# Optimization experiments

Hardware: AMD Instinct MI355X
Metric: run time of the kernel (lower is better)

The kernel has to match this reference:

```python
import jax, jax.numpy as jnp
import numpy as np

HEADS = 6
EPS = 1e-5


def _na_idx(L, k, d):
    # NATTEN-style dilated neighborhood: work within dilation cosets,
    # clamp window to stay inside the image (window shifts at borders).
    i = np.arange(L)
    g = i % d
    p = i // d
    Lg = (L - g + d - 1) // d  # coset length per position
    start = np.clip(p - k // 2, 0, Lg - k)
    j = np.arange(k)
    nbr = g[:, None] + d * (start[:, None] + j[None, :])          # [L,k] neighbor coords
    rel = (start[:, None] + j[None, :]) - p[:, None] + (k - 1)    # [L,k] rpb index in [0,2k-2]
    return jnp.asarray(nbr, jnp.int32), jnp.asarray(rel, jnp.int32)


def _na2d(x, qkv_w, qkv_b, proj_w, proj_b, rpb, heads, k, d):
    # x: [B,H,W,C] NHWC neighborhood attention with relative positional bias
    B, H, W, C = x.shape
    dh = C // heads
    scale = dh ** -0.5
    qkv = (x @ qkv_w + qkv_b).reshape(B, H, W, 3, heads, dh)
    qkv = jnp.transpose(qkv, (3, 0, 4, 1, 2, 5))  # [3,B,h,H,W,dh]
    q, kk, v = qkv[0] * scale, qkv[1], qkv[2]
    nh, rh = _na_idx(H, k, d)
    nw, rw = _na_idx(W, k, d)

    def gather(t):  # [B,h,H,W,dh] -> [B,h,H,W,k,k,dh]
        t = t[:, :, nh]              # [B,h,H,k,W,dh]
        t = t[:, :, :, :, nw]        # [B,h,H,k,W,k,dh]
        return jnp.transpose(t, (0, 1, 2, 4, 3, 5, 6))

    kn, vn = gather(kk), gather(v)
    attn = jnp.einsum('bhxyd,bhxyijd->bhxyij', q, kn)  # [B,h,H,W,k,k]
    bias = rpb[:, rh]                  # [h,H,k,2k-1]
    bias = bias[:, :, :, rw]           # [h,H,k,W,k]
    bias = jnp.transpose(bias, (0, 1, 3, 2, 4))  # [h,H,W,k,k]
    attn = attn + bias[None]
    attn = jax.nn.softmax(attn.reshape(B, heads, H, W, k * k), axis=-1)
    attn = attn.reshape(B, heads, H, W, k, k)
    out = jnp.einsum('bhxyij,bhxyijd->bhxyd', attn, vn)
    out = jnp.transpose(out, (0, 2, 3, 1, 4)).reshape(B, H, W, C)
    return out @ proj_w + proj_b


def _rln(x, w, b, m1_w, m1_b, m2_w, m2_b):
    # Revised LayerNorm: normalize over (C,H,W) per sample; meta1/meta2 are 1x1 convs on std/mean
    mean = jnp.mean(x, axis=(1, 2, 3), keepdims=True)
    std = jnp.sqrt(jnp.mean((x - mean) ** 2, axis=(1, 2, 3), keepdims=True) + EPS)
    out = (x - mean) / std * w + b
    rescale = m1_w[None, :, None, None] * std + m1_b[None, :, None, None]
    rebias = m2_w[None, :, None, None] * mean + m2_b[None, :, None, None]
    return out, rescale, rebias


def _c11(x, w, b):  # 1x1 conv on NCHW == per-pixel linear
    return jnp.einsum('bchw,oc->bohw', x, w) + b[None, :, None, None]


def _gelu(x):
    return jax.nn.gelu(x, approximate=False)


def reference(x, ln_w, ln_b, m1_w, m1_b, m2_w, m2_b, qkv1_w, qkv1_b, proj1_w, proj1_b, rpb1, qkv2_w, qkv2_b, proj2_w, proj2_b, rpb2, mlp_w1, mlp_b1, mlp_w2, mlp_b2, bn_g, bn_b, bn_m, bn_v, pa_w1, pa_b1, pa_w2, pa_b2, ca_w1, ca_b1, ca_w2, ca_b2, m2a_w1, m2a_b1, m2a_w2, m2a_b2):
    # ---- NA block 1 (kernel 7, dilation 1) ----
    sc = x
    y, rs, rb = _rln(x, ln_w, ln_b, m1_w, m1_b, m2_w, m2_b)
    a = _na2d(jnp.transpose(y, (0, 2, 3, 1)), qkv1_w, qkv1_b, proj1_w, proj1_b, rpb1, HEADS, 7, 1)
    x = sc + jnp.transpose(a, (0, 3, 1, 2)) * rs + rb
    # ---- NA block 2 (kernel 5, dilation 8) ----
    sc = x
    y, rs, rb = _rln(x, ln_w, ln_b, m1_w, m1_b, m2_w, m2_b)
    a = _na2d(jnp.transpose(y, (0, 2, 3, 1)), qkv2_w, qkv2_b, proj2_w, proj2_b, rpb2, HEADS, 5, 8)
    x = sc + jnp.transpose(a, (0, 3, 1, 2)) * rs + rb
    # ---- MLP (source reuses the pre-attn2 shortcut `sc`) ----
    y, rs, rb = _rln(x, ln_w, ln_b, m1_w, m1_b, m2_w, m2_b)
    m = _c11(jax.nn.relu(_c11(y, mlp_w1, mlp_b1)), mlp_w2, mlp_b2)
    x = sc + m * rs + rb
    # ---- BN + pixel attention + channel attention + mlp2 ----
    sc = x
    inv = jax.lax.rsqrt(bn_v + EPS)
    y = (x - bn_m[None, :, None, None]) * (inv * bn_g)[None, :, None, None] + bn_b[None, :, None, None]
    pa = jax.nn.sigmoid(_c11(_gelu(_c11(y, pa_w1, pa_b1)), pa_w2, pa_b2))  # [B,1,H,W]
    y = pa * y
    gap = jnp.mean(y, axis=(2, 3), keepdims=True)
    ca = jax.nn.sigmoid(_c11(_gelu(_c11(gap, ca_w1, ca_b1)), ca_w2, ca_b2))  # [B,C,1,1]
    y = ca * y
    y = _c11(_gelu(_c11(y, m2a_w1, m2a_b1)), m2a_w2, m2a_b2)
    return sc + y


def setup_inputs() -> dict:
    key = jax.random.key(0)
    B, C, H, W, HID = 4, 96, 64, 64, 384
    ks = iter(jax.random.split(key, 48))

    def rn(shape, s=0.02):
        return jax.random.normal(next(ks), shape, jnp.float32) * s

    d = {}
    d['x'] = jax.random.normal(next(ks), (B, C, H, W), jnp.float32)
    d['ln_w'] = jnp.ones((1, C, 1, 1), jnp.float32)
    d['ln_b'] = jnp.zeros((1, C, 1, 1), jnp.float32)
    d['m1_w'] = rn((C,)); d['m1_b'] = jnp.ones((C,), jnp.float32)
    d['m2_w'] = rn((C,)); d['m2_b'] = jnp.zeros((C,), jnp.float32)
    d['qkv1_w'] = rn((C, 3 * C)); d['qkv1_b'] = jnp.zeros((3 * C,), jnp.float32)
    d['proj1_w'] = rn((C, C)); d['proj1_b'] = jnp.zeros((C,), jnp.float32)
    d['rpb1'] = rn((HEADS, 13, 13))
    d['qkv2_w'] = rn((C, 3 * C)); d['qkv2_b'] = jnp.zeros((3 * C,), jnp.float32)
    d['proj2_w'] = rn((C, C)); d['proj2_b'] = jnp.zeros((C,), jnp.float32)
    d['rpb2'] = rn((HEADS, 9, 9))
    d['mlp_w1'] = rn((HID, C)); d['mlp_b1'] = jnp.zeros((HID,), jnp.float32)
    d['mlp_w2'] = rn((C, HID)); d['mlp_b2'] = jnp.zeros((C,), jnp.float32)
    d['bn_g'] = jnp.ones((C,), jnp.float32); d['bn_b'] = jnp.zeros((C,), jnp.float32)
    d['bn_m'] = jnp.zeros((C,), jnp.float32); d['bn_v'] = jnp.ones((C,), jnp.float32)
    d['pa_w1'] = rn((C // 8, C)); d['pa_b1'] = jnp.zeros((C // 8,), jnp.float32)
    d['pa_w2'] = rn((1, C // 8)); d['pa_b2'] = jnp.zeros((1,), jnp.float32)
    d['ca_w1'] = rn((C, C)); d['ca_b1'] = jnp.zeros((C,), jnp.float32)
    d['ca_w2'] = rn((C, C)); d['ca_b2'] = jnp.zeros((C,), jnp.float32)
    d['m2a_w1'] = rn((C, C)); d['m2a_b1'] = jnp.zeros((C,), jnp.float32)
    d['m2a_w2'] = rn((C, C)); d['m2a_b2'] = jnp.zeros((C,), jnp.float32)
    return d
```

## Files before the change

kernel.cpp:

```cpp
#include <hip/hip_runtime.h>
#include <math.h>

#define CC 96
#define NP 4096
#define NHEADS 6
#define NELEMF 393216.0f
#define EPSF 1e-5f

typedef __attribute__((ext_vector_type(8))) short bf16x8;
typedef __attribute__((ext_vector_type(4))) float f32x4;
#define MFMA16(a,b,c) __builtin_amdgcn_mfma_f32_16x16x32_bf16(a,b,c,0,0,0)

#define WQKV1  64
#define WQKV2  (WQKV1+13824)
#define WPROJ1 (WQKV2+13824)
#define WPROJ2 (WPROJ1+4608)
#define WMLP1  (WPROJ2+4608)
#define WMLP2  (WMLP1+18432)
#define WM2A1  (WMLP2+18432)
#define WM2A2  (WM2A1+4608)
#define WPA1T  (WM2A2+4608)
#define WBNS   (WPA1T+1152)
#define WS_Q   870784
#define WS_K   (WS_Q+786432)
#define WS_V   (WS_K+786432)
#define WS_ATTPM (WS_V+786432)
#define WS_X1  (WS_ATTPM+786432)
#define WS_X2  (WS_X1+1572864)
#define WS_X3  (WS_X2+1572864)
#define WS_PA  (WS_X3+1572864)
#define WS_GAP (WS_PA+16384)
#define WS_CA  (WS_GAP+384)

__device__ __forceinline__ float gelu_f(float x){
  return 0.5f * x * (1.0f + erff(x * 0.7071067811865476f));
}
__device__ __forceinline__ float sigmoid_f(float x){
  return 1.0f / (1.0f + __expf(-x));
}
__device__ __forceinline__ unsigned short bfr(float f){
  unsigned int u = __float_as_uint(f);
  u += 0x7fffu + ((u >> 16) & 1u);
  return (unsigned short)(u >> 16);
}
__device__ __forceinline__ float bflo16(unsigned short u){ return __uint_as_float(((unsigned int)u) << 16); }
__device__ __forceinline__ float bflo(unsigned int u){ return __uint_as_float(u << 16); }
__device__ __forceinline__ float bfhi(unsigned int u){ return __uint_as_float(u & 0xffff0000u); }
__device__ __forceinline__ void get_ms(const float* st, int b, float& mean, float& inv, float& stdv){
  float s = st[b], s2 = st[4+b];
  mean = s * (1.0f/NELEMF);
  float var = fmaxf(s2 * (1.0f/NELEMF) - mean*mean, 0.0f);
  stdv = sqrtf(var + EPSF);
  inv = 1.0f / stdv;
}
__device__ __forceinline__ float ldf(const float* p, int i){ return p[i]; }
__device__ __forceinline__ float ldf(const unsigned short* p, int i){ return bflo16(p[i]); }
__device__ __forceinline__ void load4(const float* p, float4& v){ v = *(const float4*)p; }
__device__ __forceinline__ void load4(const unsigned short* p, float4& v){
  ushort4 u = *(const ushort4*)p;
  v.x = bflo16(u.x); v.y = bflo16(u.y); v.z = bflo16(u.z); v.w = bflo16(u.w);
}

__global__ void prep_stats_kernel(const float* __restrict__ x, float* __restrict__ st,
                             const float* __restrict__ q1, const float* __restrict__ q2,
                             const float* __restrict__ p1, const float* __restrict__ p2,
                             const float* __restrict__ w1, const float* __restrict__ w2,
                             const float* __restrict__ a1, const float* __restrict__ a2,
                             const float* __restrict__ pw1,
                             const float* __restrict__ bg, const float* __restrict__ bb,
                             const float* __restrict__ bm, const float* __restrict__ bv,
                             float* __restrict__ ws){
  if(blockIdx.x < 384){
    int b = blockIdx.x / CC, c = blockIdx.x % CC;
    const float* p = x + (b*CC + c)*NP;
    float s = 0.f, s2 = 0.f;
    for(int i = threadIdx.x; i < NP; i += 256){ float v = p[i]; s += v; s2 = fmaf(v, v, s2); }
    for(int off = 32; off > 0; off >>= 1){ s += __shfl_down(s, off); s2 += __shfl_down(s2, off); }
    __shared__ float ls[8];
    int wid = threadIdx.x >> 6;
    if((threadIdx.x & 63) == 0){ ls[wid] = s; ls[4+wid] = s2; }
    __syncthreads();
    if(threadIdx.x == 0){
      atomicAdd(&st[b],   ls[0]+ls[1]+ls[2]+ls[3]);
      atomicAdd(&st[4+b], ls[4]+ls[5]+ls[6]+ls[7]);
    }
    return;
  }
  int gid = (blockIdx.x - 384)*256 + threadIdx.x;
  if(gid < 27648){ int n = gid/96, c = gid%96; ((unsigned short*)(ws+WQKV1))[gid] = bfr(q1[c*288+n]); }
  else if(gid < 55296){ int g = gid-27648; int n = g/96, c = g%96; ((unsigned short*)(ws+WQKV2))[g] = bfr(q2[c*288+n]); }
  else if(gid < 64512){ int g = gid-55296; int n = g/96, c = g%96; ((unsigned short*)(ws+WPROJ1))[g] = bfr(p1[c*96+n]); }
  else if(gid < 73728){ int g = gid-64512; int n = g/96, c = g%96; ((unsigned short*)(ws+WPROJ2))[g] = bfr(p2[c*96+n]); }
  else if(gid < 110592){ int g = gid-73728; ((unsigned short*)(ws+WMLP1))[g] = bfr(w1[g]); }
  else if(gid < 147456){ int g = gid-110592; ((unsigned short*)(ws+WMLP2))[g] = bfr(w2[g]); }
  else if(gid < 156672){ int g = gid-147456; ((unsigned short*)(ws+WM2A1))[g] = bfr(a1[g]); }
  else if(gid < 165888){ int g = gid-156672; ((unsigned short*)(ws+WM2A2))[g] = bfr(a2[g]); }
  else if(gid < 167040){ int g = gid-165888; int c = g/12, h = g%12; ws[WPA1T + g] = pw1[h*96+c]; }
  else if(gid < 167136){ int c = gid-167040;
    float sc = rsqrtf(bv[c] + EPSF) * bg[c];
    ws[WBNS + c] = sc;
    ws[WBNS + 96 + c] = bb[c] - bm[c]*sc;
  }
}

template<typename AT>
__global__ void __launch_bounds__(256) gemm_qkv_kernel(
    const AT* __restrict__ xin, const float* __restrict__ st,
    const float* __restrict__ lnw, const float* __restrict__ lnb,
    const unsigned short* __restrict__ wT, const float* __restrict__ qb,
    unsigned short* __restrict__ qo, unsigned short* __restrict__ ko, unsigned short* __restrict__ vo){
  __shared__ unsigned short Atl[64*104];
  __shared__ float scl[96], ofs[96];
  int m_base = blockIdx.x*64;
  int b = m_base >> 12, pxl0 = m_base & 4095;
  float mean, inv, stdv; get_ms(st, b, mean, inv, stdv);
  int tid = threadIdx.x;
  if(tid < 96){ float s = inv*lnw[tid]; scl[tid] = s; ofs[tid] = lnb[tid] - mean*s; }
  __syncthreads();
  const AT* src = xin + (size_t)b*CC*NP + pxl0;
  for(int idx = tid; idx < 96*16; idx += 256){
    int c = idx >> 4, p4 = (idx & 15) << 2;
    float4 v; load4(src + (size_t)c*NP + p4, v);
    float s = scl[c], o = ofs[c];
    Atl[(p4+0)*104 + c] = bfr(fmaf(v.x, s, o));
    Atl[(p4+1)*104 + c] = bfr(fmaf(v.y, s, o));
    Atl[(p4+2)*104 + c] = bfr(fmaf(v.z, s, o));
    Atl[(p4+3)*104 + c] = bfr(fmaf(v.w, s, o));
  }
  __syncthreads();
  int w = tid >> 6, lane = tid & 63, ml = lane & 15, q = lane >> 4;
  const unsigned short* arow = Atl + (w*16 + ml)*104;
  bf16x8 av[3];
  #pragma unroll
  for(int ks = 0; ks < 3; ++ks) av[ks] = *(const bf16x8*)(arow + ks*32 + q*8);
  f32x4 z = {0.f,0.f,0.f,0.f};
  #pragma unroll
  for(int g = 0; g < 6; ++g){
    f32x4 acc[3] = {z, z, z};
    #pragma unroll
    for(int ks = 0; ks < 3; ++ks){
      #pragma unroll
      for(int gg = 0; gg < 3; ++gg){
        bf16x8 bv = *(const bf16x8*)(wT + (g*48 + gg*16 + ml)*96 + ks*32 + q*8);
        acc[gg] = MFMA16(av[ks], bv, acc[gg]);
      }
    }
    #pragma unroll
    for(int gg = 0; gg < 3; ++gg){
      int nfb = g*48 + gg*16;
      int t = nfb/96, head = (nfb%96) >> 4;
      float scale = (t == 0) ? 0.25f : 1.0f;
      unsigned short* dst = (t == 0) ? qo : (t == 1) ? ko : vo;
      float bias = qb[nfb + ml];
      #pragma unroll
      for(int r = 0; r < 4; ++r){
        int pxl = pxl0 + w*16 + q*4 + r;
        dst[(((size_t)(b*NHEADS + head))*NP + pxl)*16 + ml] = bfr((acc[gg][r] + bias)*scale);
      }
    }
  }
}

template<typename SCT>
__global__ void __launch_bounds__(256) gemm_proj_kernel(
    const unsigned short* __restrict__ attpm, const unsigned short* __restrict__ wT,
    const float* __restrict__ pb, const SCT* __restrict__ scx, const float* __restrict__ st,
    const float* __restrict__ m1w, const float* __restrict__ m1b,
    const float* __restrict__ m2w, const float* __restrict__ m2b,
    unsigned short* __restrict__ dst, float* __restrict__ st_out){
  int w = threadIdx.x >> 6, lane = threadIdx.x & 63;
  int ml = lane & 15, q = lane >> 4;
  int m_base = blockIdx.x*128 + w*32;
  int n0 = blockIdx.y*48;
  f32x4 acc[2][3];
  f32x4 z = {0.f,0.f,0.f,0.f};
  #pragma unroll
  for(int f=0; f<2; ++f) for(int g=0; g<3; ++g) acc[f][g] = z;
  {
    const bf16x8* a0 = (const bf16x8*)(attpm + (size_t)(m_base + ml)*96 + q*8);
    const bf16x8* a1 = (const bf16x8*)(attpm + (size_t)(m_base + 16 + ml)*96 + q*8);
    #pragma unroll
    for(int ks = 0; ks < 3; ++ks){
      bf16x8 av0 = a0[ks*4], av1 = a1[ks*4];
      #pragma unroll
      for(int g = 0; g < 3; ++g){
        bf16x8 bv = *(const bf16x8*)(wT + (n0 + g*16 + ml)*96 + ks*32 + q*8);
        acc[0][g] = MFMA16(av0, bv, acc[0][g]);
        acc[1][g] = MFMA16(av1, bv, acc[1][g]);
      }
    }
  }
  __shared__ float T[48*133];
  #pragma unroll
  for(int f = 0; f < 2; ++f)
    #pragma unroll
    for(int g = 0; g < 3; ++g)
      #pragma unroll
      for(int r = 0; r < 4; ++r)
        T[(g*16 + ml)*133 + w*32 + f*16 + q*4 + r] = acc[f][g][r];
  __syncthreads();
  int b = (blockIdx.x*128) >> 12, pxl0 = (blockIdx.x*128) & 4095;
  float mean, inv, stdv; get_ms(st, b, mean, inv, stdv);
  float s = 0.f, s2 = 0.f;
  for(int idx = threadIdx.x; idx < 48*128; idx += 256){
    int row = idx >> 7, px = idx & 127;
    int n = n0 + row;
    float rsf = fmaf(m1w[n], stdv, m1b[n]);
    float rbf = fmaf(m2w[n], mean, m2b[n]);
    int ad = (b*CC + n)*NP + pxl0 + px;
    float val = ldf(scx, ad) + (T[row*133 + px] + pb[n])*rsf + rbf;
    dst[ad] = bfr(val);
    s += val; s2 = fmaf(val, val, s2);
  }
  for(int off = 32; off > 0; off >>= 1){ s += __shfl_down(s, off); s2 += __shfl_down(s2, off); }
  __shared__ float ls[8];
  int wid = threadIdx.x >> 6;
  if((threadIdx.x & 63) == 0){ ls[wid] = s; ls[4+wid] = s2; }
  __syncthreads();
  if(threadIdx.x == 0){
    atomicAdd(&st_out[b],   ls[0]+ls[1]+ls[2]+ls[3]);
    atomicAdd(&st_out[4+b], ls[4]+ls[5]+ls[6]+ls[7]);
  }
}

__global__ void __launch_bounds__(256) gemm_mlp1_kernel(
    const unsigned short* __restrict__ xin, const float* __restrict__ st,
    const float* __restrict__ lnw, const float* __restrict__ lnb,
    const unsigned short* __restrict__ wT, const float* __restrict__ b1,
    unsigned short* __restrict__ hid){
  __shared__ unsigned short Atl[64*104];
  __shared__ float scl[96], ofs[96];
  int m_base = blockIdx.x*64;
  int b = m_base >> 12, pxl0 = m_base & 4095;
  float mean, inv, stdv; get_ms(st, b, mean, inv, stdv);
  int tid = threadIdx.x;
  if(tid < 96){ float s = inv*lnw[tid]; scl[tid] = s; ofs[tid] = lnb[tid] - mean*s; }
  __syncthreads();
  const unsigned short* src = xin + (size_t)b*CC*NP + pxl0;
  for(int idx = tid; idx < 96*16; idx += 256){
    int c = idx >> 4, p4 = (idx & 15) << 2;
    float4 v; load4(src + (size_t)c*NP + p4, v);
    float s = scl[c], o = ofs[c];
    Atl[(p4+0)*104 + c] = bfr(fmaf(v.x, s, o));
    Atl[(p4+1)*104 + c] = bfr(fmaf(v.y, s, o));
    Atl[(p4+2)*104 + c] = bfr(fmaf(v.z, s, o));
    Atl[(p4+3)*104 + c] = bfr(fmaf(v.w, s, o));
  }
  __syncthreads();
  int w = tid >> 6, lane = tid & 63, ml = lane & 15, q = lane >> 4;
  const unsigned short* arow = Atl + (w*16 + ml)*104;
  bf16x8 av[3];
  #pragma unroll
  for(int ks = 0; ks < 3; ++ks) av[ks] = *(const bf16x8*)(arow + ks*32 + q*8);
  f32x4 z = {0.f,0.f,0.f,0.f};
  #pragma unroll
  for(int g = 0; g < 8; ++g){
    f32x4 acc[3] = {z, z, z};
    #pragma unroll
    for(int ks = 0; ks < 3; ++ks){
      #pragma unroll
      for(int gg = 0; gg < 3; ++gg){
        bf16x8 bv = *(const bf16x8*)(wT + (g*48 + gg*16 + ml)*96 + ks*32 + q*8);
        acc[gg] = MFMA16(av[ks], bv, acc[gg]);
      }
    }
    #pragma unroll
    for(int gg = 0; gg < 3; ++gg){
      int n = g*48 + gg*16 + ml;
      float bias = b1[n];
      #pragma unroll
      for(int r = 0; r < 4; ++r){
        int m = m_base + w*16 + q*4 + r;
        hid[(size_t)m*384 + n] = bfr(fmaxf(acc[gg][r] + bias, 0.f));
      }
    }
  }
}

__global__ void __launch_bounds__(256) gemm_mlp2_kernel(
    const unsigned short* __restrict__ hid, const unsigned short* __restrict__ wT,
    const float* __restrict__ b2, const unsigned short* __restrict__ scx, const float* __restrict__ st,
    const float* __restrict__ m1w, const float* __restrict__ m1b,
    const float* __restrict__ m2w, const float* __restrict__ m2b,
    float* __restrict__ dst){
  int w = threadIdx.x >> 6, lane = threadIdx.x & 63;
  int ml = lane & 15, q = lane >> 4;
  int m_base = blockIdx.x*128 + w*32;
  int n0 = blockIdx.y*48;
  f32x4 acc[2][3];
  f32x4 z = {0.f,0.f,0.f,0.f};
  #pragma unroll
  for(int f=0; f<2; ++f) for(int g=0; g<3; ++g) acc[f][g] = z;
  {
    const bf16x8* a0 = (const bf16x8*)(hid + (size_t)(m_base + ml)*384 + q*8);
    const bf16x8* a1 = (const bf16x8*)(hid + (size_t)(m_base + 16 + ml)*384 + q*8);
    #pragma unroll
    for(int ks = 0; ks < 12; ++ks){
      bf16x8 av0 = a0[ks*4], av1 = a1[ks*4];
      #pragma unroll
      for(int g = 0; g < 3; ++g){
        bf16x8 bv = *(const bf16x8*)(wT + (n0 + g*16 + ml)*384 + ks*32 + q*8);
        acc[0][g] = MFMA16(av0, bv, acc[0][g]);
        acc[1][g] = MFMA16(av1, bv, acc[1][g]);
      }
    }
  }
  __shared__ float T[48*133];
  #pragma unroll
  for(int f = 0; f < 2; ++f)
    #pragma unroll
    for(int g = 0; g < 3; ++g)
      #pragma unroll
      for(int r = 0; r < 4; ++r)
        T[(g*16 + ml)*133 + w*32 + f*16 + q*4 + r] = acc[f][g][r];
  __syncthreads();
  int b = (blockIdx.x*128) >> 12, pxl0 = (blockIdx.x*128) & 4095;
  float mean, inv, stdv; get_ms(st, b, mean, inv, stdv);
  for(int idx = threadIdx.x; idx < 48*128; idx += 256){
    int row = idx >> 7, px = idx & 127;
    int n = n0 + row;
    float rsf = fmaf(m1w[n], stdv, m1b[n]);
    float rbf = fmaf(m2w[n], mean, m2b[n]);
    int ad = (b*CC + n)*NP + pxl0 + px;
    dst[ad] = ldf(scx, ad) + (T[row*133 + px] + b2[n])*rsf + rbf;
  }
}

__global__ void __launch_bounds__(256) gemm_m2a_kernel(
    const float* __restrict__ x3, const float* __restrict__ bns,
    const float* __restrict__ pa, const float* __restrict__ ca,
    const unsigned short* __restrict__ w1T, const float* __restrict__ b1,
    const unsigned short* __restrict__ w2T, const float* __restrict__ b2,
    const float* __restrict__ scx, float* __restrict__ outp){
  __shared__ __align__(16) char smbuf[26624];
  __shared__ float scl[96], ofs[96], pal[64];
  unsigned short* Atl = (unsigned short*)smbuf;
  unsigned short* tl2 = (unsigned short*)(smbuf + 13312);
  float* T = (float*)smbuf;
  int m_base = blockIdx.x*64;
  int b = m_base >> 12, pxl0 = m_base & 4095;
  int tid = threadIdx.x;
  if(tid < 96){ float cv = ca[b*96 + tid]; scl[tid] = bns[tid]*cv; ofs[tid] = bns[96+tid]*cv; }
  if(tid >= 128 && tid < 192) pal[tid-128] = pa[m_base + (tid-128)];
  __syncthreads();
  const float* src = x3 + (size_t)b*CC*NP + pxl0;
  for(int idx = tid; idx < 96*16; idx += 256){
    int c = idx >> 4, p4 = (idx & 15) << 2;
    float4 v = *(const float4*)(src + (size_t)c*NP + p4);
    float s = scl[c], o = ofs[c];
    Atl[(p4+0)*104 + c] = bfr(fmaf(v.x, s, o) * pal[p4+0]);
    Atl[(p4+1)*104 + c] = bfr(fmaf(v.y, s, o) * pal[p4+1]);
    Atl[(p4+2)*104 + c] = bfr(fmaf(v.z, s, o) * pal[p4+2]);
    Atl[(p4+3)*104 + c] = bfr(fmaf(v.w, s, o) * pal[p4+3]);
  }
  __syncthreads();
  int w = tid >> 6, lane = tid & 63, ml = lane & 15, q = lane >> 4;
  f32x4 z = {0.f,0.f,0.f,0.f};
  f32x4 acc1[6];
  #pragma unroll
  for(int g=0; g<6; ++g) acc1[g] = z;
  {
    const unsigned short* arow = Atl + (w*16 + ml)*104;
    #pragma unroll
    for(int ks = 0; ks < 3; ++ks){
      bf16x8 av = *(const bf16x8*)(arow + ks*32 + q*8);
      #pragma unroll
      for(int g = 0; g < 6; ++g){
        bf16x8 bv = *(const bf16x8*)(w1T + (g*16 + ml)*96 + ks*32 + q*8);
        acc1[g] = MFMA16(av, bv, acc1[g]);
      }
    }
  }
  #pragma unroll
  for(int g = 0; g < 6; ++g){
    float bias = b1[g*16 + ml];
    #pragma unroll
    for(int r = 0; r < 4; ++r)
      tl2[(w*16 + q*4 + r)*104 + g*16 + ml] = bfr(gelu_f(acc1[g][r] + bias));
  }
  __syncthreads();
  f32x4 acc2[6];
  #pragma unroll
  for(int g=0; g<6; ++g) acc2[g] = z;
  {
    const unsigned short* arow = tl2 + (w*16 + ml)*104;
    #pragma unroll
    for(int ks = 0; ks < 3; ++ks){
      bf16x8 av = *(const bf16x8*)(arow + ks*32 + q*8);
      #pragma unroll
      for(int g = 0; g < 6; ++g){
        bf16x8 bv = *(const bf16x8*)(w2T + (g*16 + ml)*96 + ks*32 + q*8);
        acc2[g] = MFMA16(av, bv, acc2[g]);
      }
    }
  }
  __syncthreads();
  #pragma unroll
  for(int g = 0; g < 6; ++g)
    #pragma unroll
    for(int r = 0; r < 4; ++r)
      T[(g*16 + ml)*68 + w*16 + q*4 + r] = acc2[g][r];
  __syncthreads();
  for(int idx = tid; idx < 96*64; idx += 256){
    int n = idx >> 6, p = idx & 63;
    int ad = (b*CC + n)*NP + pxl0 + p;
    outp[ad] = scx[ad] + T[n*68 + p] + b2[n];
  }
}

template<int K, int D, int RPB>
__global__ void __launch_bounds__(256) attn_kernel(
    const unsigned short* __restrict__ qb, const unsigned short* __restrict__ kb,
    const unsigned short* __restrict__ vb, const float* __restrict__ rpb,
    unsigned short* __restrict__ outp){
  int bh = blockIdx.x >> 6;
  int x = blockIdx.x & 63;
  int head = bh % NHEADS, b = bh / NHEADS;

  int gx = x % D, px = x / D;
  int Lgx = (64 - gx + D - 1) / D;
  int sx = min(max(px - K/2, 0), Lgx - K);

  __shared__ unsigned int sm[2*K*512];
  unsigned int* kl = sm;
  unsigned int* vl = sm + K*512;
  const unsigned int* kg = (const unsigned int*)(kb + (size_t)bh*NP*16);
  const unsigned int* vg = (const unsigned int*)(vb + (size_t)bh*NP*16);
  int tid = threadIdx.x;
  #pragma unroll
  for(int i = 0; i < K; ++i){
    int hh = gx + D*(sx + i);
    ((uint2*)(kl + i*512))[tid] = ((const uint2*)(kg + hh*512))[tid];
    ((uint2*)(vl + i*512))[tid] = ((const uint2*)(vg + hh*512))[tid];
  }
  __syncthreads();

  int pixoff = tid >> 2, t = tid & 3;
  int y = pixoff;
  int pix = x*64 + y;
  uint2 qd = *(const uint2*)(qb + ((size_t)bh*NP + pix)*16 + 4*t);
  float qx = bflo(qd.x), qy = bfhi(qd.x), qz = bflo(qd.y), qw = bfhi(qd.y);

  int gy = y % D, py = y / D;
  int Lgy = (64 - gy + D - 1) / D;
  int sy = min(max(py - K/2, 0), Lgy - K);

  float sc[K*K];
  #pragma unroll
  for(int i = 0; i < K; ++i){
    #pragma unroll
    for(int j = 0; j < K; ++j){
      int ww = gy + D*(sy + j);
      uint2 kv = *(const uint2*)(kl + i*512 + ww*8 + t*2);
      float s = qx*bflo(kv.x);
      s = fmaf(qy, bfhi(kv.x), s);
      s = fmaf(qz, bflo(kv.y), s);
      s = fmaf(qw, bfhi(kv.y), s);
      sc[i*K + j] = s;
    }
  }
  float mx = -1e30f;
  #pragma unroll
  for(int i = 0; i < K; ++i){
    const float* brow = rpb + (head*RPB + (sx + i - px + (K-1)))*RPB + (sy - py + (K-1));
    #pragma unroll
    for(int j = 0; j < K; ++j){
      float s = sc[i*K + j];
      s += __shfl_xor(s, 1);
      s += __shfl_xor(s, 2);
      s += brow[j];
      sc[i*K + j] = s;
      mx = fmaxf(mx, s);
    }
  }
  float sum = 0.f;
  #pragma unroll
  for(int n = 0; n < K*K; ++n){ float e = __expf(sc[n] - mx); sc[n] = e; sum += e; }
  float rs = 1.0f / sum;
  float4 acc = {0,0,0,0};
  #pragma unroll
  for(int i = 0; i < K; ++i){
    #pragma unroll
    for(int j = 0; j < K; ++j){
      int ww = gy + D*(sy + j);
      float wgt = sc[i*K + j] * rs;
      uint2 vv = *(const uint2*)(vl + i*512 + ww*8 + t*2);
      acc.x = fmaf(wgt, bflo(vv.x), acc.x);
      acc.y = fmaf(wgt, bfhi(vv.x), acc.y);
      acc.z = fmaf(wgt, bflo(vv.y), acc.z);
      acc.w = fmaf(wgt, bfhi(vv.y), acc.w);
    }
  }
  ushort4 o4;
  o4.x = bfr(acc.x); o4.y = bfr(acc.y); o4.z = bfr(acc.z); o4.w = bfr(acc.w);
  *(ushort4*)(outp + ((size_t)(b*NP + pix))*96 + head*16 + 4*t) = o4;
}

__global__ void __launch_bounds__(256) pa_kernel(
    const float* __restrict__ x3, const float* __restrict__ bns,
    const float* __restrict__ w1t, const float* __restrict__ b1,
    const float* __restrict__ w2, const float* __restrict__ b2,
    float* __restrict__ pa){
  int b = blockIdx.x >> 6;
  int px0 = (blockIdx.x & 63)*64;
  int pxq = threadIdx.x >> 2, t = threadIdx.x & 3;
  int p = px0 + pxq;
  float acc[12];
  #pragma unroll
  for(int h = 0; h < 12; ++h) acc[h] = 0.f;
  #pragma unroll 6
  for(int cc = 0; cc < 24; ++cc){
    int c = t*24 + cc;
    float yv = fmaf(x3[(b*CC + c)*NP + p], bns[c], bns[96 + c]);
    #pragma unroll
    for(int h = 0; h < 12; ++h) acc[h] = fmaf(yv, w1t[c*12 + h], acc[h]);
  }
  #pragma unroll
  for(int h = 0; h < 12; ++h){
    acc[h] += __shfl_xor(acc[h], 1);
    acc[h] += __shfl_xor(acc[h], 2);
  }
  float s = b2[0];
  #pragma unroll
  for(int h = 0; h < 12; ++h) s = fmaf(gelu_f(acc[h] + b1[h]), w2[h], s);
  if(t == 0) pa[b*NP + p] = sigmoid_f(s);
}

__global__ void gap_kernel(const float* __restrict__ x3, const float* __restrict__ bns,
                           const float* __restrict__ pa, float* __restrict__ gap){
  int b = blockIdx.x / CC, c = blockIdx.x % CC;
  float scb = bns[c], shb = bns[96 + c];
  float s = 0.f;
  for(int i = threadIdx.x; i < NP; i += 256)
    s = fmaf(fmaf(x3[(b*CC + c)*NP + i], scb, shb), pa[b*NP + i], s);
  for(int off = 32; off > 0; off >>= 1) s += __shfl_down(s, off);
  __shared__ float ls[4];
  if((threadIdx.x & 63) == 0) ls[threadIdx.x >> 6] = s;
  __syncthreads();
  if(threadIdx.x == 0) gap[blockIdx.x] = (ls[0]+ls[1]+ls[2]+ls[3]) * (1.0f/4096.0f);
}

__global__ void ca_kernel(const float* __restrict__ gap, const float* __restrict__ w1,
                          const float* __restrict__ b1, const float* __restrict__ w2,
                          const float* __restrict__ b2, float* __restrict__ ca){
  int b = blockIdx.x; int o = threadIdx.x;
  __shared__ float g[96], t[96];
  if(o < 96) g[o] = gap[b*96 + o];
  __syncthreads();
  if(o < 96){
    float a = b1[o];
    for(int c = 0; c < 96; ++c) a = fmaf(g[c], w1[o*96 + c], a);
    t[o] = gelu_f(a);
  }
  __syncthreads();
  if(o < 96){
    float a = b2[o];
    for(int c = 0; c < 96; ++c) a = fmaf(t[c], w2[o*96 + c], a);
    ca[b*96 + o] = sigmoid_f(a);
  }
}

extern "C" void kernel_launch(void* const* d_in, const int* in_sizes, int n_in,
                              void* d_out, int out_size, void* d_ws, size_t ws_size,
                              hipStream_t stream){
  (void)in_sizes; (void)n_in; (void)out_size; (void)ws_size;
  const float* x     = (const float*)d_in[0];
  const float* lnw   = (const float*)d_in[1];
  const float* lnb   = (const float*)d_in[2];
  const float* m1w   = (const float*)d_in[3];
  const float* m1b   = (const float*)d_in[4];
  const float* m2w   = (const float*)d_in[5];
  const float* m2b   = (const float*)d_in[6];
  const float* qkv1w = (const float*)d_in[7];
  const float* qkv1b = (const float*)d_in[8];
  const float* proj1w= (const float*)d_in[9];
  const float* proj1b= (const float*)d_in[10];
  const float* rpb1  = (const float*)d_in[11];
  const float* qkv2w = (const float*)d_in[12];
  const float* qkv2b = (const float*)d_in[13];
  const float* proj2w= (const float*)d_in[14];
  const float* proj2b= (const float*)d_in[15];
  const float* rpb2  = (const float*)d_in[16];
  const float* mw1   = (const float*)d_in[17];
  const float* mb1   = (const float*)d_in[18];
  const float* mw2   = (const float*)d_in[19];
  const float* mb2   = (const float*)d_in[20];
  const float* bng   = (const float*)d_in[21];
  const float* bnb   = (const float*)d_in[22];
  const float* bnm   = (const float*)d_in[23];
  const float* bnv   = (const float*)d_in[24];
  const float* paw1  = (const float*)d_in[25];
  const float* pab1  = (const float*)d_in[26];
  const float* paw2  = (const float*)d_in[27];
  const float* pab2  = (const float*)d_in[28];
  const float* caw1  = (const float*)d_in[29];
  const float* cab1  = (const float*)d_in[30];
  const float* caw2  = (const float*)d_in[31];
  const float* cab2  = (const float*)d_in[32];
  const float* aw1   = (const float*)d_in[33];
  const float* ab1   = (const float*)d_in[34];
  const float* aw2   = (const float*)d_in[35];
  const float* ab2   = (const float*)d_in[36];

  float* ws  = (float*)d_ws;
  float* out = (float*)d_out;
  float* st0 = ws;
  float* st1 = ws + 8;
  float* st2 = ws + 16;
  unsigned short* q     = (unsigned short*)(ws + WS_Q);
  unsigned short* k     = (unsigned short*)(ws + WS_K);
  unsigned short* v     = (unsigned short*)(ws + WS_V);
  unsigned short* attpm = (unsigned short*)(ws + WS_ATTPM);
  unsigned short* hid   = (unsigned short*)(ws + WS_Q);
  unsigned short* x1b   = (unsigned short*)(ws + WS_X1);
  unsigned short* x2b   = (unsigned short*)(ws + WS_X2);
  float* x3  = ws + WS_X3;
  float* pab = ws + WS_PA;
  float* gpb = ws + WS_GAP;
  float* cab = ws + WS_CA;
  float* bns = ws + WBNS;

  hipMemsetAsync(d_ws, 0, 64*sizeof(float), stream);
  prep_stats_kernel<<<1040, 256, 0, stream>>>(x, st0, qkv1w, qkv2w, proj1w, proj2w,
                                              mw1, mw2, aw1, aw2, paw1,
                                              bng, bnb, bnm, bnv, ws);

  gemm_qkv_kernel<float><<<256, 256, 0, stream>>>(x, st0, lnw, lnb,
      (unsigned short*)(ws+WQKV1), qkv1b, q, k, v);
  attn_kernel<7,1,13><<<1536, 256, 0, stream>>>(q, k, v, rpb1, attpm);
  gemm_proj_kernel<float><<<dim3(128,2), 256, 0, stream>>>(attpm, (unsigned short*)(ws+WPROJ1),
      proj1b, x, st0, m1w, m1b, m2w, m2b, x1b, st1);

  gemm_qkv_kernel<unsigned short><<<256, 256, 0, stream>>>(x1b, st1, lnw, lnb,
      (unsigned short*)(ws+WQKV2), qkv2b, q, k, v);
  attn_kernel<5,8,9><<<1536, 256, 0, stream>>>(q, k, v, rpb2, attpm);
  gemm_proj_kernel<unsigned short><<<dim3(128,2), 256, 0, stream>>>(attpm, (unsigned short*)(ws+WPROJ2),
      proj2b, x1b, st1, m1w, m1b, m2w, m2b, x2b, st2);

  gemm_mlp1_kernel<<<256, 256, 0, stream>>>(x2b, st2, lnw, lnb,
      (unsigned short*)(ws+WMLP1), mb1, hid);
  gemm_mlp2_kernel<<<dim3(128,2), 256, 0, stream>>>(hid, (unsigned short*)(ws+WMLP2), mb2,
      x1b, st2, m1w, m1b, m2w, m2b, x3);

  pa_kernel<<<256, 256, 0, stream>>>(x3, bns, ws + WPA1T, pab1, paw2, pab2, pab);
  gap_kernel<<<384, 256, 0, stream>>>(x3, bns, pab, gpb);
  ca_kernel<<<4, 128, 0, stream>>>(gpb, caw1, cab1, caw2, cab2, cab);
  gemm_m2a_kernel<<<256, 256, 0, stream>>>(x3, bns, pab, cab, (unsigned short*)(ws+WM2A1), ab1,
                                           (unsigned short*)(ws+WM2A2), ab2, x3, out);
}
```

Measured before the change: 294.0 us.

## Fuse MLP GEMMs via shared-memory hidden tile and merge PA with GAP

```diff
diff --git a/kernel.cpp b/kernel.cpp
--- a/kernel.cpp
+++ b/kernel.cpp
@@ -101,6 +101,7 @@
     ws[WBNS + c] = sc;
     ws[WBNS + 96 + c] = bb[c] - bm[c]*sc;
   }
+  else if(gid < 167520){ ws[WS_GAP + (gid-167136)] = 0.f; }
 }
 
 template<typename AT>
@@ -223,13 +224,20 @@
   }
 }
 
-__global__ void __launch_bounds__(256) gemm_mlp1_kernel(
+__global__ void __launch_bounds__(256) gemm_mlp_kernel(
     const unsigned short* __restrict__ xin, const float* __restrict__ st,
     const float* __restrict__ lnw, const float* __restrict__ lnb,
-    const unsigned short* __restrict__ wT, const float* __restrict__ b1,
-    unsigned short* __restrict__ hid){
-  __shared__ unsigned short Atl[64*104];
+    const unsigned short* __restrict__ w1T, const float* __restrict__ b1,
+    const unsigned short* __restrict__ w2T, const float* __restrict__ b2,
+    const unsigned short* __restrict__ scx,
+    const float* __restrict__ m1w, const float* __restrict__ m1b,
+    const float* __restrict__ m2w, const float* __restrict__ m2b,
+    float* __restrict__ dst){
+  __shared__ __align__(16) char smbuf[63488];
   __shared__ float scl[96], ofs[96];
+  unsigned short* Atl  = (unsigned short*)smbuf;
+  unsigned short* hidL = (unsigned short*)(smbuf + 13312);
+  float* T = (float*)(smbuf + 13312);
   int m_base = blockIdx.x*64;
   int b = m_base >> 12, pxl0 = m_base & 4095;
   float mean, inv, stdv; get_ms(st, b, mean, inv, stdv);
@@ -248,81 +256,62 @@
   }
   __syncthreads();
   int w = tid >> 6, lane = tid & 63, ml = lane & 15, q = lane >> 4;
-  const unsigned short* arow = Atl + (w*16 + ml)*104;
-  bf16x8 av[3];
-  #pragma unroll
-  for(int ks = 0; ks < 3; ++ks) av[ks] = *(const bf16x8*)(arow + ks*32 + q*8);
   f32x4 z = {0.f,0.f,0.f,0.f};
-  #pragma unroll
-  for(int g = 0; g < 8; ++g){
-    f32x4 acc[3] = {z, z, z};
-    #pragma unroll
-    for(int ks = 0; ks < 3; ++ks){
+  {
+    const unsigned short* arow = Atl + (w*16 + ml)*104;
+    bf16x8 av[3];
+    #pragma unroll
+    for(int ks = 0; ks < 3; ++ks) av[ks] = *(const bf16x8*)(arow + ks*32 + q*8);
+    #pragma unroll
+    for(int g = 0; g < 8; ++g){
+      f32x4 acc[3] = {z, z, z};
+      #pragma unroll
+      for(int ks = 0; ks < 3; ++ks){
+        #pragma unroll
+        for(int gg = 0; gg < 3; ++gg){
+          bf16x8 bv = *(const bf16x8*)(w1T + (g*48 + gg*16 + ml)*96 + ks*32 + q*8);
+          acc[gg] = MFMA16(av[ks], bv, acc[gg]);
+        }
+      }
       #pragma unroll
       for(int gg = 0; gg < 3; ++gg){
-        bf16x8 bv = *(const bf16x8*)(wT + (g*48 + gg*16 + ml)*96 + ks*32 + q*8);
-        acc[gg] = MFMA16(av[ks], bv, acc[gg]);
-      }
-    }
-    #pragma unroll
-    for(int gg = 0; gg < 3; ++gg){
-      int n = g*48 + gg*16 + ml;
-      float bias = b1[n];
-      #pragma unroll
-      for(int r = 0; r < 4; ++r){
-        int m = m_base + w*16 + q*4 + r;
-        hid[(size_t)m*384 + n] = bfr(fmaxf(acc[gg][r] + bias, 0.f));
-      }
-    }
-  }
-}
-
-__global__ void __launch_bounds__(256) gemm_mlp2_kernel(
-    const unsigned short* __restrict__ hid, const unsigned short* __restrict__ wT,
-    const float* __restrict__ b2, const unsigned short* __restrict__ scx, const float* __restrict__ st,
-    const float* __restrict__ m1w, const float* __restrict__ m1b,
-    const float* __restrict__ m2w, const float* __restrict__ m2b,
-    float* __restrict__ dst){
-  int w = threadIdx.x >> 6, lane = threadIdx.x & 63;
-  int ml = lane & 15, q = lane >> 4;
-  int m_base = blockIdx.x*128 + w*32;
-  int n0 = blockIdx.y*48;
-  f32x4 acc[2][3];
-  f32x4 z = {0.f,0.f,0.f,0.f};
-  #pragma unroll
-  for(int f=0; f<2; ++f) for(int g=0; g<3; ++g) acc[f][g] = z;
+        int n = g*48 + gg*16 + ml;
+        float bias = b1[n];
+        #pragma unroll
+        for(int r = 0; r < 4; ++r)
+          hidL[(w*16 + q*4 + r)*392 + n] = bfr(fmaxf(acc[gg][r] + bias, 0.f));
+      }
+    }
+  }
+  __syncthreads();
+  f32x4 acc2[6];
+  #pragma unroll
+  for(int g=0; g<6; ++g) acc2[g] = z;
   {
-    const bf16x8* a0 = (const bf16x8*)(hid + (size_t)(m_base + ml)*384 + q*8);
-    const bf16x8* a1 = (const bf16x8*)(hid + (size_t)(m_base + 16 + ml)*384 + q*8);
+    const unsigned short* arow = hidL + (w*16 + ml)*392;
     #pragma unroll
     for(int ks = 0; ks < 12; ++ks){
-      bf16x8 av0 = a0[ks*4], av1 = a1[ks*4];
-      #pragma unroll
-      for(int g = 0; g < 3; ++g){
-        bf16x8 bv = *(const bf16x8*)(wT + (n0 + g*16 + ml)*384 + ks*32 + q*8);
-        acc[0][g] = MFMA16(av0, bv, acc[0][g]);
-        acc[1][g] = MFMA16(av1, bv, acc[1][g]);
-      }
-    }
-  }
-  __shared__ float T[48*133];
-  #pragma unroll
-  for(int f = 0; f < 2; ++f)
-    #pragma unroll
-    for(int g = 0; g < 3; ++g)
-      #pragma unroll
-      for(int r = 0; r < 4; ++r)
-        T[(g*16 + ml)*133 + w*32 + f*16 + q*4 + r] = acc[f][g][r];
-  __syncthreads();
-  int b = (blockIdx.x*128) >> 12, pxl0 = (blockIdx.x*128) & 4095;
-  float mean, inv, stdv; get_ms(st, b, mean, inv, stdv);
-  for(int idx = threadIdx.x; idx < 48*128; idx += 256){
-    int row = idx >> 7, px = idx & 127;
-    int n = n0 + row;
+      bf16x8 av = *(const bf16x8*)(arow + ks*32 + q*8);
+      #pragma unroll
+      for(int g = 0; g < 6; ++g){
+        bf16x8 bv = *(const bf16x8*)(w2T + (g*16 + ml)*384 + ks*32 + q*8);
+        acc2[g] = MFMA16(av, bv, acc2[g]);
+      }
+    }
+  }
+  __syncthreads();
+  #pragma unroll
+  for(int g = 0; g < 6; ++g)
+    #pragma unroll
+    for(int r = 0; r < 4; ++r)
+      T[(g*16 + ml)*68 + w*16 + q*4 + r] = acc2[g][r];
+  __syncthreads();
+  for(int idx = tid; idx < 96*64; idx += 256){
+    int n = idx >> 6, px = idx & 63;
     float rsf = fmaf(m1w[n], stdv, m1b[n]);
     float rbf = fmaf(m2w[n], mean, m2b[n]);
     int ad = (b*CC + n)*NP + pxl0 + px;
-    dst[ad] = ldf(scx, ad) + (T[row*133 + px] + b2[n])*rsf + rbf;
+    dst[ad] = ldf(scx, ad) + (T[n*68 + px] + b2[n])*rsf + rbf;
   }
 }
 
@@ -496,15 +485,16 @@
   *(ushort4*)(outp + ((size_t)(b*NP + pix))*96 + head*16 + 4*t) = o4;
 }
 
-__global__ void __launch_bounds__(256) pa_kernel(
+__global__ void __launch_bounds__(256) pa_gap_kernel(
     const float* __restrict__ x3, const float* __restrict__ bns,
     const float* __restrict__ w1t, const float* __restrict__ b1,
     const float* __restrict__ w2, const float* __restrict__ b2,
-    float* __restrict__ pa){
+    float* __restrict__ pa, float* __restrict__ gap){
   int b = blockIdx.x >> 6;
   int px0 = (blockIdx.x & 63)*64;
   int pxq = threadIdx.x >> 2, t = threadIdx.x & 3;
   int p = px0 + pxq;
+  float yvv[24];
   float acc[12];
   #pragma unroll
   for(int h = 0; h < 12; ++h) acc[h] = 0.f;
@@ -512,6 +502,7 @@
   for(int cc = 0; cc < 24; ++cc){
     int c = t*24 + cc;
     float yv = fmaf(x3[(b*CC + c)*NP + p], bns[c], bns[96 + c]);
+    yvv[cc] = yv;
     #pragma unroll
     for(int h = 0; h < 12; ++h) acc[h] = fmaf(yv, w1t[c*12 + h], acc[h]);
   }
@@ -523,21 +514,23 @@
   float s = b2[0];
   #pragma unroll
   for(int h = 0; h < 12; ++h) s = fmaf(gelu_f(acc[h] + b1[h]), w2[h], s);
-  if(t == 0) pa[b*NP + p] = sigmoid_f(s);
-}
-
-__global__ void gap_kernel(const float* __restrict__ x3, const float* __restrict__ bns,
-                           const float* __restrict__ pa, float* __restrict__ gap){
-  int b = blockIdx.x / CC, c = blockIdx.x % CC;
-  float scb = bns[c], shb = bns[96 + c];
-  float s = 0.f;
-  for(int i = threadIdx.x; i < NP; i += 256)
-    s = fmaf(fmaf(x3[(b*CC + c)*NP + i], scb, shb), pa[b*NP + i], s);
-  for(int off = 32; off > 0; off >>= 1) s += __shfl_down(s, off);
-  __shared__ float ls[4];
-  if((threadIdx.x & 63) == 0) ls[threadIdx.x >> 6] = s;
-  __syncthreads();
-  if(threadIdx.x == 0) gap[blockIdx.x] = (ls[0]+ls[1]+ls[2]+ls[3]) * (1.0f/4096.0f);
+  float pav = sigmoid_f(s);
+  if(t == 0) pa[b*NP + p] = pav;
+  __shared__ float gpart[4*96];
+  int w = threadIdx.x >> 6, lane = threadIdx.x & 63;
+  #pragma unroll 6
+  for(int cc = 0; cc < 24; ++cc){
+    float g = yvv[cc] * pav;
+    g += __shfl_xor(g, 4);  g += __shfl_xor(g, 8);
+    g += __shfl_xor(g, 16); g += __shfl_xor(g, 32);
+    if(lane < 4 && lane == t) gpart[w*96 + t*24 + cc] = g;
+  }
+  __syncthreads();
+  if(threadIdx.x < 96){
+    int c = threadIdx.x;
+    float v = (gpart[c] + gpart[96+c] + gpart[192+c] + gpart[288+c]) * (1.0f/4096.0f);
+    atomicAdd(&gap[b*96 + c], v);
+  }
 }
 
 __global__ void ca_kernel(const float* __restrict__ gap, const float* __restrict__ w1,
@@ -611,7 +604,6 @@
   unsigned short* k     = (unsigned short*)(ws + WS_K);
   unsigned short* v     = (unsigned short*)(ws + WS_V);
   unsigned short* attpm = (unsigned short*)(ws + WS_ATTPM);
-  unsigned short* hid   = (unsigned short*)(ws + WS_Q);
   unsigned short* x1b   = (unsigned short*)(ws + WS_X1);
   unsigned short* x2b   = (unsigned short*)(ws + WS_X2);
   float* x3  = ws + WS_X3;
@@ -637,13 +629,11 @@
   gemm_proj_kernel<unsigned short><<<dim3(128,2), 256, 0, stream>>>(attpm, (unsigned short*)(ws+WPROJ2),
       proj2b, x1b, st1, m1w, m1b, m2w, m2b, x2b, st2);
 
-  gemm_mlp1_kernel<<<256, 256, 0, stream>>>(x2b, st2, lnw, lnb,
-      (unsigned short*)(ws+WMLP1), mb1, hid);
-  gemm_mlp2_kernel<<<dim3(128,2), 256, 0, stream>>>(hid, (unsigned short*)(ws+WMLP2), mb2,
-      x1b, st2, m1w, m1b, m2w, m2b, x3);
-
-  pa_kernel<<<256, 256, 0, stream>>>(x3, bns, ws + WPA1T, pab1, paw2, pab2, pab);
-  gap_kernel<<<384, 256, 0, stream>>>(x3, bns, pab, gpb);
+  gemm_mlp_kernel<<<256, 256, 0, stream>>>(x2b, st2, lnw, lnb,
+      (unsigned short*)(ws+WMLP1), mb1, (unsigned short*)(ws+WMLP2), mb2,
+      x1b, m1w, m1b, m2w, m2b, x3);
+
+  pa_gap_kernel<<<256, 256, 0, stream>>>(x3, bns, ws + WPA1T, pab1, paw2, pab2, pab, gpb);
   ca_kernel<<<4, 128, 0, stream>>>(gpb, caw1, cab1, caw2, cab2, cab);
   gemm_m2a_kernel<<<256, 256, 0, stream>>>(x3, bns, pab, cab, (unsigned short*)(ws+WM2A1), ab1,
                                            (unsigned short*)(ws+WM2A2), ab2, x3, out);
```

Measured after the change: 291.0 us. About the same (-1.0%).
